# Optimization experiments

Hardware: AMD Instinct MI355X
Metric: run time of the kernel (lower is better)

Reference implementation:

```python
import jax, jax.numpy as jnp
import numpy as np

N_FEATURES = 16384
N_EXPERTS = 8
D_IN = 768
EXPERT_DIM = N_FEATURES // N_EXPERTS  # 2048
N_TOKENS = 16384


def setup_inputs() -> dict:
    key = jax.random.key(0)
    k_act, k_preb, k_enc, k_dec, k_rb, k_r = jax.random.split(key, 6)
    activations = jax.random.normal(k_act, (N_TOKENS, D_IN), dtype=jnp.float32)
    pre_b = jax.random.normal(k_preb, (D_IN,), dtype=jnp.float32) * 0.01
    enc = jax.random.normal(k_enc, (N_EXPERTS, D_IN, EXPERT_DIM), dtype=jnp.float32) / (2.0 ** 0.5) / (D_IN ** 0.5)
    dec = jax.random.normal(k_dec, (N_EXPERTS, EXPERT_DIM, D_IN), dtype=jnp.float32) / (EXPERT_DIM ** 0.5)
    router_b = jax.random.normal(k_rb, (D_IN,), dtype=jnp.float32) * 0.01
    router = jax.random.normal(k_r, (D_IN, N_EXPERTS), dtype=jnp.float32) / (D_IN ** 0.5)
    return {"activations": activations, "pre_b": pre_b, "enc": enc, "dec": dec,
            "router_b": router_b, "router": router}


def reference(activations, pre_b, enc, dec, router_b, router):
    # Router: softmax over experts, top-1 routing.
    logits = (activations - router_b) @ router            # [N, E]
    probs = jax.nn.softmax(logits, axis=-1)
    expert_max_prob = jnp.max(probs, axis=-1)              # [N]
    expert_idx = jnp.argmax(probs, axis=-1)                # [N] int

    n_experts = enc.shape[0]
    recons = jnp.zeros_like(activations)
    # Fixed small loop over experts; tokens are masked (zeroed) per expert so
    # each per-expert encode/decode GEMM only contributes for its routed rows.
    for e in range(n_experts):
        mask = (expert_idx == e)[:, None]                  # [N, 1]
        x_e = jnp.where(mask, activations, 0.0)            # masked gather
        latent = jax.nn.relu(x_e @ enc[e])                 # [N, expert_dim]
        recon = latent @ dec[e]                            # [N, d_in]
        recons = recons + jnp.where(mask, recon, 0.0)      # scatter-combine

    return expert_max_prob[:, None] * recons + pre_b
```

## Files before the change

kernel.cpp:

```cpp
#include <hip/hip_runtime.h>
#include <hip/hip_bf16.h>
#include <hip/hip_fp16.h>

#define N_TOKENS 16384
#define D_IN 768
#define N_EXPERTS 8
#define EXPERT_DIM 2048

#define ROUTER_BLOCKS 256
#define TOK_PER_BLOCK 64

typedef _Float16 half8 __attribute__((ext_vector_type(8)));
typedef _Float16 half4 __attribute__((ext_vector_type(4)));
typedef float floatx4 __attribute__((ext_vector_type(4)));


#define WAIT_VM12 0xF7C
#define WAIT_VM8  0xF78
#define WAIT_VM4  0xF74
#define WAIT_VM0  0xF70

__device__ __forceinline__ void glds16(const _Float16* g, _Float16* l) {
    __builtin_amdgcn_global_load_lds(
        (const __attribute__((address_space(1))) unsigned int*)g,
        (__attribute__((address_space(3))) unsigned int*)l, 16, 0, 0);
}

__global__ __launch_bounds__(256) void router_convert(const float* __restrict__ act,
    const float* __restrict__ router_b, const float* __restrict__ router,
    _Float16* __restrict__ act_h, float* __restrict__ prob, int* __restrict__ localpos,
    int* __restrict__ eidx, int* __restrict__ hist)
{
    __shared__ int h[N_EXPERTS];
    if (threadIdx.x < N_EXPERTS) h[threadIdx.x] = 0;
    __syncthreads();

    int wave = threadIdx.x >> 6, lane = threadIdx.x & 63;

    float rb[3][4];
#pragma unroll
    for (int c = 0; c < 3; ++c) {
        float4 v = *(const float4*)(router_b + lane * 4 + c * 256);
        rb[c][0] = v.x; rb[c][1] = v.y; rb[c][2] = v.z; rb[c][3] = v.w;
    }

#pragma unroll 1
    for (int it = 0; it < 16; ++it) {
        int t = blockIdx.x * TOK_PER_BLOCK + wave * 16 + it;
        const float* arow = act + (size_t)t * D_IN;
        float acc[8];
#pragma unroll
        for (int e = 0; e < 8; ++e) acc[e] = 0.f;
#pragma unroll
        for (int c = 0; c < 3; ++c) {
            int i0 = lane * 4 + c * 256;
            float4 v = *(const float4*)(arow + i0);
            half4 hv;
            hv[0] = (_Float16)v.x; hv[1] = (_Float16)v.y;
            hv[2] = (_Float16)v.z; hv[3] = (_Float16)v.w;
            *(half4*)(act_h + (size_t)t * D_IN + i0) = hv;
            float va[4] = {v.x, v.y, v.z, v.w};
#pragma unroll
            for (int q = 0; q < 4; ++q) {
                float a = va[q] - rb[c][q];
                const float* r = router + (size_t)(i0 + q) * 8;
#pragma unroll
                for (int e = 0; e < 8; ++e) acc[e] += a * r[e];
            }
        }
#pragma unroll
        for (int s = 32; s > 0; s >>= 1) {
#pragma unroll
            for (int e = 0; e < 8; ++e) acc[e] += __shfl_down(acc[e], s, 64);
        }
        if (lane == 0) {
            float m = acc[0]; int ai = 0;
#pragma unroll
            for (int e = 1; e < 8; ++e) if (acc[e] > m) { m = acc[e]; ai = e; }
            float s = 0.f;
#pragma unroll
            for (int e = 0; e < 8; ++e) s += __expf(acc[e] - m);
            prob[t] = 1.0f / s;
            eidx[t] = ai;
            localpos[t] = atomicAdd(&h[ai], 1);
        }
    }
    __syncthreads();
    if (threadIdx.x < N_EXPERTS) hist[blockIdx.x * N_EXPERTS + threadIdx.x] = h[threadIdx.x];
}

__global__ __launch_bounds__(256) void scan_kernel(int* __restrict__ hist,
    int* __restrict__ counts, int* __restrict__ offsets)
{
    __shared__ int sh[ROUTER_BLOCKS * N_EXPERTS];
    __shared__ int tot[N_EXPERTS], off[N_EXPERTS];
    int tid = threadIdx.x;
    *(int4*)&sh[tid * 8]     = *(const int4*)&hist[tid * 8];
    *(int4*)&sh[tid * 8 + 4] = *(const int4*)&hist[tid * 8 + 4];
    __syncthreads();
    if (tid < N_EXPERTS) {
        int run = 0;
        for (int b = 0; b < ROUTER_BLOCKS; ++b) {
            int v = sh[b * 8 + tid];
            sh[b * 8 + tid] = run;
            run += v;
        }
        tot[tid] = run;
    }
    __syncthreads();
    if (tid == 0) {
        int run = 0;
        for (int e = 0; e < N_EXPERTS; ++e) {
            off[e] = run; offsets[e] = run; counts[e] = tot[e]; run += tot[e];
        }
    }
    __syncthreads();
    int4 a = *(const int4*)&sh[tid * 8];
    int4 b = *(const int4*)&sh[tid * 8 + 4];
    a.x += off[0]; a.y += off[1]; a.z += off[2]; a.w += off[3];
    b.x += off[4]; b.y += off[5]; b.z += off[6]; b.w += off[7];
    *(int4*)&hist[tid * 8]     = a;
    *(int4*)&hist[tid * 8 + 4] = b;
}

__global__ __launch_bounds__(256) void order_kernel(const int* __restrict__ eidx,
    const int* __restrict__ localpos, const int* __restrict__ hist,
    int* __restrict__ order)
{
    int t = blockIdx.x * 256 + threadIdx.x;
    int base = hist[(t >> 6) * N_EXPERTS + eidx[t]];
    order[base + localpos[t]] = t;
}

__global__ __launch_bounds__(256) void transpose_to_half(const float* __restrict__ W,
    _Float16* __restrict__ WT, int K, int Nc)
{
    __shared__ _Float16 tile[64][72];
    size_t esz = (size_t)K * Nc;
    const float* We = W + (size_t)blockIdx.z * esz;
    _Float16* WTe = WT + (size_t)blockIdx.z * esz;
    int n0 = blockIdx.x * 64, k0 = blockIdx.y * 64;
    int tr = threadIdx.x >> 4;
    int tc = threadIdx.x & 15;
#pragma unroll
    for (int rr = 0; rr < 64; rr += 16) {
        int k = k0 + rr + tr;
        float4 v = *(const float4*)(We + (size_t)k * Nc + n0 + tc * 4);
        tile[tc * 4 + 0][rr + tr] = (_Float16)v.x;
        tile[tc * 4 + 1][rr + tr] = (_Float16)v.y;
        tile[tc * 4 + 2][rr + tr] = (_Float16)v.z;
        tile[tc * 4 + 3][rr + tr] = (_Float16)v.w;
    }
    __syncthreads();
#pragma unroll
    for (int p = 0; p < 2; ++p) {
        int id = threadIdx.x + p * 256;
        int r = id >> 3, ch = id & 7;
        half8 v = *(const half8*)&tile[r][ch * 8];
        *(half8*)(WTe + (size_t)(n0 + r) * K + k0 + ch * 8) = v;
    }
}

#define STAGE(bufp, k0h)                                        \
    do {                                                        \
        glds16(pa0 + (k0h), (bufp) + st_base);                  \
        glds16(pa1 + (k0h), (bufp) + st_base + 512);            \
        glds16(pb0 + (k0h), (bufp) + 8192 + st_base);           \
        glds16(pb1 + (k0h), (bufp) + 8192 + st_base + 512);     \
    } while (0)

__global__ __launch_bounds__(512, 2) void encode_kernel(const _Float16* __restrict__ act_h,
    const _Float16* __restrict__ encT, const int* __restrict__ order,
    const int* __restrict__ counts, const int* __restrict__ offsets,
    _Float16* __restrict__ latent)
{
    int id = blockIdx.x;
    int e = id & 7;
    int j = id >> 3;
    int nt = j & 7;
    int mt = j >> 3;

    int n_e = counts[e];
    if (mt * 256 >= n_e) return;
    int slot0 = offsets[e] + mt * 256;
    int mrem = n_e - mt * 256;

    __shared__ _Float16 lds[4][16384];
    __shared__ int s_tok[256];

    int tid = threadIdx.x;
    if (tid < 256) s_tok[tid] = (tid < mrem) ? order[slot0 + tid] : order[slot0];
    __syncthreads();

    int w = tid >> 6, lane = tid & 63;
    int wm = w >> 2, wn = w & 3;
    int mrow = lane & 15;

    int st_base = w * 1024 + lane * 8;
    int c_st = ((lane & 3) - ((lane >> 3) & 3)) & 3;
    int r_in = lane >> 2;
    const _Float16* Be = encT + (size_t)e * D_IN * EXPERT_DIM + (size_t)(nt * 256) * D_IN;
    const _Float16* pa0 = act_h + (size_t)s_tok[w * 32 + r_in] * D_IN + c_st * 8;
    const _Float16* pa1 = act_h + (size_t)s_tok[w * 32 + 16 + r_in] * D_IN + c_st * 8;
    const _Float16* pb0 = Be + (size_t)(w * 32 + r_in) * D_IN + c_st * 8;
    const _Float16* pb1 = Be + (size_t)(w * 32 + 16 + r_in) * D_IN + c_st * 8;

    int fo = (((lane >> 4) + (mrow >> 1)) & 3) * 8;
    int aoff = (wm * 128 + mrow) * 32 + fo;
    int boff = 8192 + (wn * 64 + mrow) * 32 + fo;

    floatx4 acc[8][4];
#pragma unroll
    for (int i = 0; i < 8; ++i)
#pragma unroll
        for (int jj = 0; jj < 4; ++jj) acc[i][jj] = (floatx4){0.f, 0.f, 0.f, 0.f};

    const int T = D_IN / 32;
    STAGE(&lds[0][0], 0);
    STAGE(&lds[1][0], 32);
    STAGE(&lds[2][0], 64);

#pragma unroll 1
    for (int t = 0; t < T; ++t) {
        _Float16* cur = &lds[t & 3][0];
        if (t + 3 < T) {
            STAGE(&lds[(t + 3) & 3][0], (t + 3) * 32);
            __builtin_amdgcn_s_waitcnt(WAIT_VM12);
        } else if (t + 2 < T) {
            __builtin_amdgcn_s_waitcnt(WAIT_VM8);
        } else if (t + 1 < T) {
            __builtin_amdgcn_s_waitcnt(WAIT_VM4);
        } else {
            __builtin_amdgcn_s_waitcnt(WAIT_VM0);
        }
        __builtin_amdgcn_s_barrier();
        half8 af[8], bf[4];
#pragma unroll
        for (int i = 0; i < 8; ++i) af[i] = *(const half8*)&cur[aoff + i * 512];
#pragma unroll
        for (int jj = 0; jj < 4; ++jj) bf[jj] = *(const half8*)&cur[boff + jj * 512];
        __builtin_amdgcn_s_setprio(1);
#pragma unroll
        for (int i = 0; i < 8; ++i)
#pragma unroll
            for (int jj = 0; jj < 4; ++jj)
                acc[i][jj] = __builtin_amdgcn_mfma_f32_16x16x32_f16(af[i], bf[jj], acc[i][jj], 0, 0, 0);
        __builtin_amdgcn_s_setprio(0);
        __builtin_amdgcn_s_barrier();
    }

#pragma unroll
    for (int i = 0; i < 8; ++i) {
        int row0 = wm * 128 + i * 16 + (lane >> 4) * 4;
#pragma unroll
        for (int jj = 0; jj < 4; ++jj) {
            int col = nt * 256 + wn * 64 + jj * 16 + mrow;
#pragma unroll
            for (int r = 0; r < 4; ++r) {
                int row = row0 + r;
                if (row < mrem) {
                    float v = acc[i][jj][r];
                    v = v > 0.f ? v : 0.f;
                    latent[(size_t)(slot0 + row) * EXPERT_DIM + col] = (_Float16)v;
                }
            }
        }
    }
}

__global__ __launch_bounds__(512, 2) void decode_kernel(const _Float16* __restrict__ latent,
    const _Float16* __restrict__ decT, const int* __restrict__ order,
    const int* __restrict__ counts, const int* __restrict__ offsets,
    const float* __restrict__ prob, const float* __restrict__ pre_b,
    float* __restrict__ out)
{
    int id = blockIdx.x;
    int e = id & 7;
    int j = id >> 3;
    int nt = j % 3;
    int mt = j / 3;

    int n_e = counts[e];
    if (mt * 256 >= n_e) return;
    int slot0 = offsets[e] + mt * 256;
    int mrem = n_e - mt * 256;

    __shared__ _Float16 lds[4][16384];
    __shared__ int s_tok[256];
    __shared__ float s_p[256];

    int tid = threadIdx.x;
    if (tid < 256) {
        int tok = (tid < mrem) ? order[slot0 + tid] : order[slot0];
        s_tok[tid] = tok;
        s_p[tid] = prob[tok];
    }
    __syncthreads();

    int w = tid >> 6, lane = tid & 63;
    int wm = w >> 2, wn = w & 3;
    int mrow = lane & 15;

    int st_base = w * 1024 + lane * 8;
    int c_st = ((lane & 3) - ((lane >> 3) & 3)) & 3;
    int r_in = lane >> 2;
    const _Float16* Ae = latent + (size_t)slot0 * EXPERT_DIM;
    const _Float16* Be = decT + (size_t)e * EXPERT_DIM * D_IN + (size_t)(nt * 256) * EXPERT_DIM;
    const _Float16* pa0 = Ae + (size_t)(w * 32 + r_in) * EXPERT_DIM + c_st * 8;
    const _Float16* pa1 = Ae + (size_t)(w * 32 + 16 + r_in) * EXPERT_DIM + c_st * 8;
    const _Float16* pb0 = Be + (size_t)(w * 32 + r_in) * EXPERT_DIM + c_st * 8;
    const _Float16* pb1 = Be + (size_t)(w * 32 + 16 + r_in) * EXPERT_DIM + c_st * 8;

    int fo = (((lane >> 4) + (mrow >> 1)) & 3) * 8;
    int aoff = (wm * 128 + mrow) * 32 + fo;
    int boff = 8192 + (wn * 64 + mrow) * 32 + fo;

    floatx4 acc[8][4];
#pragma unroll
    for (int i = 0; i < 8; ++i)
#pragma unroll
        for (int jj = 0; jj < 4; ++jj) acc[i][jj] = (floatx4){0.f, 0.f, 0.f, 0.f};

    const int T = EXPERT_DIM / 32;
    STAGE(&lds[0][0], 0);
    STAGE(&lds[1][0], 32);
    STAGE(&lds[2][0], 64);

#pragma unroll 1
    for (int t = 0; t < T; ++t) {
        _Float16* cur = &lds[t & 3][0];
        if (t + 3 < T) {
            STAGE(&lds[(t + 3) & 3][0], (t + 3) * 32);
            __builtin_amdgcn_s_waitcnt(WAIT_VM12);
        } else if (t + 2 < T) {
            __builtin_amdgcn_s_waitcnt(WAIT_VM8);
        } else if (t + 1 < T) {
            __builtin_amdgcn_s_waitcnt(WAIT_VM4);
        } else {
            __builtin_amdgcn_s_waitcnt(WAIT_VM0);
        }
        __builtin_amdgcn_s_barrier();
        half8 af[8], bf[4];
#pragma unroll
        for (int i = 0; i < 8; ++i) af[i] = *(const half8*)&cur[aoff + i * 512];
#pragma unroll
        for (int jj = 0; jj < 4; ++jj) bf[jj] = *(const half8*)&cur[boff + jj * 512];
        __builtin_amdgcn_s_setprio(1);
#pragma unroll
        for (int i = 0; i < 8; ++i)
#pragma unroll
            for (int jj = 0; jj < 4; ++jj)
                acc[i][jj] = __builtin_amdgcn_mfma_f32_16x16x32_f16(af[i], bf[jj], acc[i][jj], 0, 0, 0);
        __builtin_amdgcn_s_setprio(0);
        __builtin_amdgcn_s_barrier();
    }

#pragma unroll
    for (int i = 0; i < 8; ++i) {
        int row0 = wm * 128 + i * 16 + (lane >> 4) * 4;
#pragma unroll
        for (int jj = 0; jj < 4; ++jj) {
            int col = nt * 256 + wn * 64 + jj * 16 + mrow;
            float pb = pre_b[col];
#pragma unroll
            for (int r = 0; r < 4; ++r) {
                int row = row0 + r;
                if (row < mrem) {
                    out[(size_t)s_tok[row] * D_IN + col] = s_p[row] * acc[i][jj][r] + pb;
                }
            }
        }
    }
}

extern "C" void kernel_launch(void* const* d_in, const int* in_sizes, int n_in,
                              void* d_out, int out_size, void* d_ws, size_t ws_size,
                              hipStream_t stream)
{
    const float* act      = (const float*)d_in[0];
    const float* pre_b    = (const float*)d_in[1];
    const float* enc      = (const float*)d_in[2];
    const float* dec      = (const float*)d_in[3];
    const float* router_b = (const float*)d_in[4];
    const float* router   = (const float*)d_in[5];
    float* out = (float*)d_out;

    char* w = (char*)d_ws;
    int* counts  = (int*)w;  w += 256;
    int* offsets = (int*)w;  w += 256;
    int* hist    = (int*)w;  w += ROUTER_BLOCKS * N_EXPERTS * 4;
    int* eidx    = (int*)w;  w += N_TOKENS * 4;
    int* lpos    = (int*)w;  w += N_TOKENS * 4;
    int* order   = (int*)w;  w += N_TOKENS * 4;
    float* prob  = (float*)w; w += N_TOKENS * 4;
    _Float16* act_h  = (_Float16*)w; w += (size_t)N_TOKENS * D_IN * 2;
    _Float16* encT   = (_Float16*)w; w += (size_t)N_EXPERTS * D_IN * EXPERT_DIM * 2;
    _Float16* decT   = (_Float16*)w; w += (size_t)N_EXPERTS * D_IN * EXPERT_DIM * 2;
    _Float16* latent = (_Float16*)w; w += (size_t)(N_TOKENS + 256) * EXPERT_DIM * 2;

    router_convert<<<ROUTER_BLOCKS, 256, 0, stream>>>(act, router_b, router, act_h, prob, lpos, eidx, hist);
    scan_kernel<<<1, 256, 0, stream>>>(hist, counts, offsets);
    order_kernel<<<N_TOKENS / 256, 256, 0, stream>>>(eidx, lpos, hist, order);

    transpose_to_half<<<dim3(EXPERT_DIM / 64, D_IN / 64, N_EXPERTS), 256, 0, stream>>>(enc, encT, D_IN, EXPERT_DIM);
    transpose_to_half<<<dim3(D_IN / 64, EXPERT_DIM / 64, N_EXPERTS), 256, 0, stream>>>(dec, decT, EXPERT_DIM, D_IN);

    encode_kernel<<<4096, 512, 0, stream>>>(act_h, encT, order, counts, offsets, latent);
    decode_kernel<<<1536, 512, 0, stream>>>(latent, decT, order, counts, offsets, prob, pre_b, out);
}
```

Baseline: 391.0 us.

## Interleave split A/B tile staging with two MFMA halves and merge transpose launches

The encode and decode GEMM main loops now split each K-step into two halves. The prefetch of A and the prefetch of B for step t+3 are issued between the two MFMA halves, and the vmcnt wait plus barrier move to the end of the iteration, so global-to-LDS loads are spread across the compute. This is meant to smooth memory issue and hide load latency behind the matrix work, at the cost of extra barriers per iteration. The two weight transpose launches are also merged into one grid to save a kernel launch.

```diff
diff --git a/kernel.cpp b/kernel.cpp
--- a/kernel.cpp
+++ b/kernel.cpp
@@ -15,7 +15,6 @@
 typedef float floatx4 __attribute__((ext_vector_type(4)));
 
 
-#define WAIT_VM12 0xF7C
 #define WAIT_VM8  0xF78
 #define WAIT_VM4  0xF74
 #define WAIT_VM0  0xF70
@@ -132,14 +131,24 @@
     order[base + localpos[t]] = t;
 }
 
-__global__ __launch_bounds__(256) void transpose_to_half(const float* __restrict__ W,
-    _Float16* __restrict__ WT, int K, int Nc)
+__global__ __launch_bounds__(256) void transpose_both(const float* __restrict__ enc,
+    const float* __restrict__ dec, _Float16* __restrict__ encT, _Float16* __restrict__ decT)
 {
     __shared__ _Float16 tile[64][72];
+    int id = blockIdx.x;
+    const float* W; _Float16* WT; int K, Nc, bx, by, bz;
+    if (id < 3072) {
+        W = enc; WT = encT; K = D_IN; Nc = EXPERT_DIM;
+        bx = id & 31; by = (id >> 5) % 12; bz = id / 384;
+    } else {
+        int id2 = id - 3072;
+        W = dec; WT = decT; K = EXPERT_DIM; Nc = D_IN;
+        bx = id2 % 12; by = (id2 / 12) & 31; bz = id2 / 384;
+    }
     size_t esz = (size_t)K * Nc;
-    const float* We = W + (size_t)blockIdx.z * esz;
-    _Float16* WTe = WT + (size_t)blockIdx.z * esz;
-    int n0 = blockIdx.x * 64, k0 = blockIdx.y * 64;
+    const float* We = W + (size_t)bz * esz;
+    _Float16* WTe = WT + (size_t)bz * esz;
+    int n0 = bx * 64, k0 = by * 64;
     int tr = threadIdx.x >> 4;
     int tc = threadIdx.x & 15;
 #pragma unroll
@@ -154,17 +163,20 @@
     __syncthreads();
 #pragma unroll
     for (int p = 0; p < 2; ++p) {
-        int id = threadIdx.x + p * 256;
-        int r = id >> 3, ch = id & 7;
+        int idp = threadIdx.x + p * 256;
+        int r = idp >> 3, ch = idp & 7;
         half8 v = *(const half8*)&tile[r][ch * 8];
         *(half8*)(WTe + (size_t)(n0 + r) * K + k0 + ch * 8) = v;
     }
 }
 
-#define STAGE(bufp, k0h)                                        \
+#define STAGE_A(bufp, k0h)                                      \
     do {                                                        \
         glds16(pa0 + (k0h), (bufp) + st_base);                  \
         glds16(pa1 + (k0h), (bufp) + st_base + 512);            \
+    } while (0)
+#define STAGE_B(bufp, k0h)                                      \
+    do {                                                        \
         glds16(pb0 + (k0h), (bufp) + 8192 + st_base);           \
         glds16(pb1 + (k0h), (bufp) + 8192 + st_base + 512);     \
     } while (0)
@@ -216,37 +228,50 @@
         for (int jj = 0; jj < 4; ++jj) acc[i][jj] = (floatx4){0.f, 0.f, 0.f, 0.f};
 
     const int T = D_IN / 32;
-    STAGE(&lds[0][0], 0);
-    STAGE(&lds[1][0], 32);
-    STAGE(&lds[2][0], 64);
+    STAGE_A(&lds[0][0], 0);  STAGE_B(&lds[0][0], 0);
+    STAGE_A(&lds[1][0], 32); STAGE_B(&lds[1][0], 32);
+    STAGE_A(&lds[2][0], 64); STAGE_B(&lds[2][0], 64);
+    __builtin_amdgcn_s_waitcnt(WAIT_VM8);
+    __builtin_amdgcn_s_barrier();
 
 #pragma unroll 1
     for (int t = 0; t < T; ++t) {
         _Float16* cur = &lds[t & 3][0];
-        if (t + 3 < T) {
-            STAGE(&lds[(t + 3) & 3][0], (t + 3) * 32);
-            __builtin_amdgcn_s_waitcnt(WAIT_VM12);
-        } else if (t + 2 < T) {
-            __builtin_amdgcn_s_waitcnt(WAIT_VM8);
-        } else if (t + 1 < T) {
-            __builtin_amdgcn_s_waitcnt(WAIT_VM4);
-        } else {
-            __builtin_amdgcn_s_waitcnt(WAIT_VM0);
-        }
-        __builtin_amdgcn_s_barrier();
-        half8 af[8], bf[4];
-#pragma unroll
-        for (int i = 0; i < 8; ++i) af[i] = *(const half8*)&cur[aoff + i * 512];
+        _Float16* nx3 = &lds[(t + 3) & 3][0];
+        int k3 = (t + 3) * 32;
+        half8 af0[4], bf[4];
+#pragma unroll
+        for (int i = 0; i < 4; ++i) af0[i] = *(const half8*)&cur[aoff + i * 512];
 #pragma unroll
         for (int jj = 0; jj < 4; ++jj) bf[jj] = *(const half8*)&cur[boff + jj * 512];
+        if (t + 3 < T) STAGE_A(nx3, k3);
+        __builtin_amdgcn_s_barrier();
         __builtin_amdgcn_s_setprio(1);
 #pragma unroll
-        for (int i = 0; i < 8; ++i)
+        for (int i = 0; i < 4; ++i)
 #pragma unroll
             for (int jj = 0; jj < 4; ++jj)
-                acc[i][jj] = __builtin_amdgcn_mfma_f32_16x16x32_f16(af[i], bf[jj], acc[i][jj], 0, 0, 0);
+                acc[i][jj] = __builtin_amdgcn_mfma_f32_16x16x32_f16(af0[i], bf[jj], acc[i][jj], 0, 0, 0);
         __builtin_amdgcn_s_setprio(0);
         __builtin_amdgcn_s_barrier();
+        half8 af1[4];
+#pragma unroll
+        for (int i = 0; i < 4; ++i) af1[i] = *(const half8*)&cur[aoff + (i + 4) * 512];
+        if (t + 3 < T) STAGE_B(nx3, k3);
+        __builtin_amdgcn_s_barrier();
+        __builtin_amdgcn_s_setprio(1);
+#pragma unroll
+        for (int i = 0; i < 4; ++i)
+#pragma unroll
+            for (int jj = 0; jj < 4; ++jj)
+                acc[i + 4][jj] = __builtin_amdgcn_mfma_f32_16x16x32_f16(af1[i], bf[jj], acc[i + 4][jj], 0, 0, 0);
+        __builtin_amdgcn_s_setprio(0);
+        if (t + 1 < T) {
+            if (t + 3 < T)      __builtin_amdgcn_s_waitcnt(WAIT_VM8);
+            else if (t + 2 < T) __builtin_amdgcn_s_waitcnt(WAIT_VM4);
+            else                __builtin_amdgcn_s_waitcnt(WAIT_VM0);
+            __builtin_amdgcn_s_barrier();
+        }
     }
 
 #pragma unroll
@@ -322,37 +347,50 @@
         for (int jj = 0; jj < 4; ++jj) acc[i][jj] = (floatx4){0.f, 0.f, 0.f, 0.f};
 
     const int T = EXPERT_DIM / 32;
-    STAGE(&lds[0][0], 0);
-    STAGE(&lds[1][0], 32);
-    STAGE(&lds[2][0], 64);
+    STAGE_A(&lds[0][0], 0);  STAGE_B(&lds[0][0], 0);
+    STAGE_A(&lds[1][0], 32); STAGE_B(&lds[1][0], 32);
+    STAGE_A(&lds[2][0], 64); STAGE_B(&lds[2][0], 64);
+    __builtin_amdgcn_s_waitcnt(WAIT_VM8);
+    __builtin_amdgcn_s_barrier();
 
 #pragma unroll 1
     for (int t = 0; t < T; ++t) {
         _Float16* cur = &lds[t & 3][0];
-        if (t + 3 < T) {
-            STAGE(&lds[(t + 3) & 3][0], (t + 3) * 32);
-            __builtin_amdgcn_s_waitcnt(WAIT_VM12);
-        } else if (t + 2 < T) {
-            __builtin_amdgcn_s_waitcnt(WAIT_VM8);
-        } else if (t + 1 < T) {
-            __builtin_amdgcn_s_waitcnt(WAIT_VM4);
-        } else {
-            __builtin_amdgcn_s_waitcnt(WAIT_VM0);
-        }
-        __builtin_amdgcn_s_barrier();
-        half8 af[8], bf[4];
-#pragma unroll
-        for (int i = 0; i < 8; ++i) af[i] = *(const half8*)&cur[aoff + i * 512];
+        _Float16* nx3 = &lds[(t + 3) & 3][0];
+        int k3 = (t + 3) * 32;
+        half8 af0[4], bf[4];
+#pragma unroll
+        for (int i = 0; i < 4; ++i) af0[i] = *(const half8*)&cur[aoff + i * 512];
 #pragma unroll
         for (int jj = 0; jj < 4; ++jj) bf[jj] = *(const half8*)&cur[boff + jj * 512];
+        if (t + 3 < T) STAGE_A(nx3, k3);
+        __builtin_amdgcn_s_barrier();
         __builtin_amdgcn_s_setprio(1);
 #pragma unroll
-        for (int i = 0; i < 8; ++i)
+        for (int i = 0; i < 4; ++i)
 #pragma unroll
             for (int jj = 0; jj < 4; ++jj)
-                acc[i][jj] = __builtin_amdgcn_mfma_f32_16x16x32_f16(af[i], bf[jj], acc[i][jj], 0, 0, 0);
+                acc[i][jj] = __builtin_amdgcn_mfma_f32_16x16x32_f16(af0[i], bf[jj], acc[i][jj], 0, 0, 0);
         __builtin_amdgcn_s_setprio(0);
         __builtin_amdgcn_s_barrier();
+        half8 af1[4];
+#pragma unroll
+        for (int i = 0; i < 4; ++i) af1[i] = *(const half8*)&cur[aoff + (i + 4) * 512];
+        if (t + 3 < T) STAGE_B(nx3, k3);
+        __builtin_amdgcn_s_barrier();
+        __builtin_amdgcn_s_setprio(1);
+#pragma unroll
+        for (int i = 0; i < 4; ++i)
+#pragma unroll
+            for (int jj = 0; jj < 4; ++jj)
+                acc[i + 4][jj] = __builtin_amdgcn_mfma_f32_16x16x32_f16(af1[i], bf[jj], acc[i + 4][jj], 0, 0, 0);
+        __builtin_amdgcn_s_setprio(0);
+        if (t + 1 < T) {
+            if (t + 3 < T)      __builtin_amdgcn_s_waitcnt(WAIT_VM8);
+            else if (t + 2 < T) __builtin_amdgcn_s_waitcnt(WAIT_VM4);
+            else                __builtin_amdgcn_s_waitcnt(WAIT_VM0);
+            __builtin_amdgcn_s_barrier();
+        }
     }
 
 #pragma unroll
@@ -402,8 +440,7 @@
     scan_kernel<<<1, 256, 0, stream>>>(hist, counts, offsets);
     order_kernel<<<N_TOKENS / 256, 256, 0, stream>>>(eidx, lpos, hist, order);
 
-    transpose_to_half<<<dim3(EXPERT_DIM / 64, D_IN / 64, N_EXPERTS), 256, 0, stream>>>(enc, encT, D_IN, EXPERT_DIM);
-    transpose_to_half<<<dim3(D_IN / 64, EXPERT_DIM / 64, N_EXPERTS), 256, 0, stream>>>(dec, decT, EXPERT_DIM, D_IN);
+    transpose_both<<<6144, 256, 0, stream>>>(enc, dec, encT, decT);
 
     encode_kernel<<<4096, 512, 0, stream>>>(act_h, encT, order, counts, offsets, latent);
     decode_kernel<<<1536, 512, 0, stream>>>(latent, decT, order, counts, offsets, prob, pre_b, out);
```

Result: faster. 370.7 us (-5.2%).
